# Optimization experiments

Measured on AMD Instinct MI355X. Metric: run time of the kernel, lower is better.

Reference implementation:

```python
import jax, jax.numpy as jnp
import numpy as np

E, IN, OUT, T = 8, 4096, 4096, 8192
GS = IN  # groupsize=-1 -> groupsize = infeatures


def setup_inputs() -> dict:
    key = jax.random.key(0)
    k1, k2, k3, k4, k5 = jax.random.split(key, 5)
    x = jax.random.normal(k1, (T, IN), dtype=jnp.float16)
    indices = jax.random.randint(k2, (T,), 0, E, dtype=jnp.int32)
    # int32 words each packing 8 int4 nonzero values (2:4 sparse -> IN*OUT/2 values per expert)
    qweight = jax.random.randint(k3, (E, IN // 32, OUT * 16 // 8), 0, 2**31 - 1, dtype=jnp.int32)
    meta = jax.random.randint(k4, (E, OUT, IN // 16), 0, 2**15, dtype=jnp.int32).astype(jnp.int16)
    scales = (jax.random.uniform(k5, (E, IN // GS, OUT), dtype=jnp.float32) * 0.02 + 0.001).astype(jnp.float16)
    return {"x": x, "indices": indices, "qweight": qweight, "meta": meta, "scales": scales}


def _dequant_24(qweight, meta, scales):
    """Decode packed int4 + 2:4-sparsity metadata into dense fp32 weights (E, OUT, IN)."""
    # unpack 8 int4 nibbles per int32 word, symmetric zero-point 8
    nib = (qweight[..., None] >> (4 * jnp.arange(8, dtype=jnp.int32))) & 0xF  # (E, IN//32, 2*OUT, 8)
    vals = nib.reshape(E, IN // 2, OUT).transpose(0, 2, 1).astype(jnp.float32) - 8.0  # (E, OUT, IN//2)
    m = meta.astype(jnp.int32) & 0xFFFF
    sub = (m[..., None] >> (2 * jnp.arange(8, dtype=jnp.int32))) & 0x3  # (E, OUT, IN//16, 8)
    grp = (jnp.arange(8, dtype=jnp.int32) // 2) * 4                      # group-of-4 base within 16-block
    base = 16 * jnp.arange(IN // 16, dtype=jnp.int32)                    # 16-block base
    dense_col = (base[None, None, :, None] + grp[None, None, None, :] + sub).reshape(E, OUT, IN // 2)
    eidx = jnp.arange(E)[:, None, None]
    oidx = jnp.arange(OUT)[None, :, None]
    W = jnp.zeros((E, OUT, IN), jnp.float32).at[eidx, oidx, dense_col].add(vals)
    # per-group dequant scales: (E, IN//GS, OUT) -> (E, OUT, IN)
    s = jnp.repeat(scales.astype(jnp.float32), GS, axis=1).transpose(0, 2, 1)
    return W * s


def reference(x, indices, qweight, meta, scales):
    W = _dequant_24(qweight, meta, scales)  # (E, OUT, IN)
    y = jnp.zeros((x.shape[0], OUT), jnp.float32)
    for e in range(E):  # fixed small expert count
        xe = jnp.where((indices == e)[:, None], x, 0).astype(jnp.float32)
        y = y + xe @ W[e].T
    return y.astype(x.dtype)
```

## Files before the change

### kernel.cpp

```cpp
#include <hip/hip_runtime.h>

#define E_N   8
#define IN_N  4096
#define OUT_N 4096
#define T_N   8192

#define BM 128
#define BN 256
#define BK 64
#define NTHREADS 512

typedef unsigned short u16;
typedef __bf16 bf16_t;
typedef bf16_t bf16x8 __attribute__((ext_vector_type(8)));
typedef u16    u16x8  __attribute__((ext_vector_type(8)));
typedef float  f32x4  __attribute__((ext_vector_type(4)));

#define GLOAD16(gsrc, ldst) \
    __builtin_amdgcn_global_load_lds( \
        (const __attribute__((address_space(1))) unsigned int*)(gsrc), \
        (__attribute__((address_space(3))) unsigned int*)(ldst), 16, 0, 0)

__device__ int g_cnt[E_N];
__device__ int g_base[E_N];
__device__ int g_ids[T_N];
__device__ int g_meta_wide;
__device__ u16 g_W[(long)E_N * OUT_N * IN_N];
__device__ u16 g_xb[(long)T_N * IN_N];

__device__ __forceinline__ u16 f2bf(float f) {
    unsigned u = __builtin_bit_cast(unsigned, f);
    u += 0x7FFFu + ((u >> 16) & 1u);
    return (u16)(u >> 16);
}

__global__ void sort_tokens(const int* __restrict__ idx, const u16* __restrict__ meta16) {
    __shared__ int cnt[E_N], off[E_N];
    __shared__ int probe;
    const int tid = threadIdx.x;
    const int lane = tid & 63;
    if (tid == 0) probe = 0;
    if (tid < E_N) cnt[tid] = 0;
    __syncthreads();
    if (tid < 64) {
        unsigned v = meta16[2 * (tid * 131072) + 1];
        if (v) atomicOr(&probe, 1);
    }
    for (int t0 = tid - lane; t0 < T_N; t0 += blockDim.x) {
        const int t = t0 + lane;
        const int my = idx[t] & 7;
        #pragma unroll
        for (int e = 0; e < E_N; ++e) {
            unsigned long long m = __ballot(my == e);
            if (lane == 0 && m) atomicAdd(&cnt[e], __popcll(m));
        }
    }
    __syncthreads();
    if (tid == 0) {
        int s = 0;
        for (int e = 0; e < E_N; ++e) { g_cnt[e] = cnt[e]; g_base[e] = s; off[e] = s; s += cnt[e]; }
        g_meta_wide = (probe == 0) ? 1 : 0;
    }
    __syncthreads();
    for (int t0 = tid - lane; t0 < T_N; t0 += blockDim.x) {
        const int t = t0 + lane;
        const int my = idx[t] & 7;
        #pragma unroll
        for (int e = 0; e < E_N; ++e) {
            unsigned long long m = __ballot(my == e);
            if (my == e) {
                int below = __popcll(m & ((1ull << lane) - 1ull));
                int basep = 0;
                if (below == 0) basep = atomicAdd(&off[e], __popcll(m));
                int src = __ffsll((long long)m) - 1;
                basep = __shfl(basep, src);
                int p = basep + below;
                if (p >= 0 && p < T_N) g_ids[p] = t;
            }
        }
    }
}

__global__ __launch_bounds__(256, 4)
void xb_convert(const float* __restrict__ x) {
    const int p = blockIdx.x;
    int tok = g_ids[p];
    if ((unsigned)tok >= (unsigned)T_N) tok = 0;
    const float* src = x + (long)tok * IN_N;
    u16* dst = g_xb + (long)p * IN_N;
    const int tid = threadIdx.x;
    float va[16];
    #pragma unroll
    for (int c4 = 0; c4 < 4; ++c4) {
        float4 v = *reinterpret_cast<const float4*>(src + tid * 16 + c4 * 4);
        va[c4 * 4 + 0] = v.x; va[c4 * 4 + 1] = v.y; va[c4 * 4 + 2] = v.z; va[c4 * 4 + 3] = v.w;
    }
    unsigned wp[8];
    #pragma unroll
    for (int p8 = 0; p8 < 8; ++p8)
        wp[p8] = (unsigned)f2bf(va[2 * p8]) | ((unsigned)f2bf(va[2 * p8 + 1]) << 16);
    *reinterpret_cast<int4*>(dst + tid * 16)     = make_int4((int)wp[0], (int)wp[1], (int)wp[2], (int)wp[3]);
    *reinterpret_cast<int4*>(dst + tid * 16 + 8) = make_int4((int)wp[4], (int)wp[5], (int)wp[6], (int)wp[7]);
}

__global__ __launch_bounds__(256, 4)
void decode_w(const int* __restrict__ qw, const void* __restrict__ meta) {
    const int e   = blockIdx.z;
    const int kt0 = blockIdx.y * 4;
    const int o   = blockIdx.x * 256 + threadIdx.x;
    const bool mwide = (g_meta_wide != 0);
    unsigned mws[16];
    if (mwide) {
        const int* mp = (const int*)meta + ((long)e * OUT_N + o) * (IN_N / 16) + kt0 * 4;
        #pragma unroll
        for (int i = 0; i < 16; ++i) mws[i] = (unsigned)mp[i] & 0xFFFFu;
    } else {
        const u16* mp = (const u16*)meta + ((long)e * OUT_N + o) * (IN_N / 16) + kt0 * 4;
        #pragma unroll
        for (int i = 0; i < 16; ++i) mws[i] = mp[i];
    }
    const unsigned sh = (o & 7) << 2;
    const int osw = o & 7;
    #pragma unroll
    for (int ki = 0; ki < 4; ++ki) {
        const int kt = kt0 + ki;
        unsigned wp[32];
        #pragma unroll
        for (int gi = 0; gi < 4; ++gi) {
            const int g = kt * 4 + gi;
            const unsigned mw = mws[ki * 4 + gi];
            const int* qp = qw + ((e * (IN_N / 32) + (g >> 1)) << 13) + (o >> 3) + ((g & 1) << 12);
            int d[16];
            #pragma unroll
            for (int p = 0; p < 16; ++p) d[p] = 0;
            #pragma unroll
            for (int grp = 0; grp < 4; ++grp) {
                const unsigned w0 = (unsigned)qp[(2 * grp) * 512];
                const unsigned w1 = (unsigned)qp[(2 * grp + 1) * 512];
                const int v0 = (int)((w0 >> sh) & 0xF) - 8;
                const int v1 = (int)((w1 >> sh) & 0xF) - 8;
                const int s0 = (mw >> (4 * grp)) & 3;
                const int s1 = (mw >> (4 * grp + 2)) & 3;
                #pragma unroll
                for (int q = 0; q < 4; ++q) {
                    int t0 = (s0 == q) ? v0 : 0;
                    int t1 = (s1 == q) ? v1 : 0;
                    d[grp * 4 + q] = t0 + t1;
                }
            }
            #pragma unroll
            for (int p = 0; p < 8; ++p) {
                unsigned lo = __builtin_bit_cast(unsigned, (float)d[2 * p])     >> 16;
                unsigned hi = __builtin_bit_cast(unsigned, (float)d[2 * p + 1]) >> 16;
                wp[gi * 8 + p] = lo | (hi << 16);
            }
        }
        u16* wr = g_W + ((long)(e * 64 + kt) * OUT_N + o) * 64;
        #pragma unroll
        for (int h = 0; h < 8; ++h)
            *reinterpret_cast<int4*>(wr + (h ^ osw) * 8) =
                make_int4((int)wp[h * 4], (int)wp[h * 4 + 1], (int)wp[h * 4 + 2], (int)wp[h * 4 + 3]);
    }
}

__global__ __launch_bounds__(NTHREADS, 1)
void moe_gemm(const float* __restrict__ scales, float* __restrict__ y) {
    const int e = blockIdx.z;
    int cnt = g_cnt[e];
    if (cnt < 0) cnt = 0;
    if (cnt > T_N) cnt = T_N;
    const int m0 = blockIdx.y * BM;
    if (m0 >= cnt) return;
    const int n0 = blockIdx.x * BN;
    int base = g_base[e];
    if (base < 0) base = 0;
    if (base > T_N - cnt) base = T_N - cnt;

    __shared__ __align__(16) u16 As[BM * BK];
    __shared__ __align__(16) u16 Bs[BN * BK];

    const int tid  = threadIdx.x;
    const int lane = tid & 63;
    const int wm   = (tid >> 6) >> 2;
    const int wn   = (tid >> 6) & 3;

    const int r0 = tid >> 3;
    const int kc_swz = (tid & 7) ^ (r0 & 7);
    long ar0 = (long)base + m0 + r0;       if (ar0 > T_N - 1) ar0 = T_N - 1;
    long ar1 = (long)base + m0 + 64 + r0;  if (ar1 > T_N - 1) ar1 = T_N - 1;
    const u16* asrc0 = g_xb + ar0 * IN_N + kc_swz * 8;
    const u16* asrc1 = g_xb + ar1 * IN_N + kc_swz * 8;
    u16* adst0 = &As[tid * 8];
    u16* adst1 = &As[(tid + 512) * 8];
    const u16* bsrc = g_W + ((long)e * 64 * OUT_N + n0) * 64 + tid * 8;

    f32x4 acc[4][4];
    #pragma unroll
    for (int i = 0; i < 4; ++i)
        #pragma unroll
        for (int j = 0; j < 4; ++j) acc[i][j] = (f32x4){0.f, 0.f, 0.f, 0.f};

    for (int k0 = 0; k0 < IN_N; k0 += BK) {
        GLOAD16(asrc0 + k0, adst0);
        GLOAD16(asrc1 + k0, adst1);
        #pragma unroll
        for (int it = 0; it < 4; ++it)
            GLOAD16(bsrc + it * 4096, &Bs[(tid + it * 512) * 8]);
        bsrc += (long)OUT_N * 64;
        __syncthreads();
        #pragma unroll
        for (int kk = 0; kk < BK; kk += 32) {
            bf16x8 af[4], bfr[4];
            #pragma unroll
            for (int mf = 0; mf < 4; ++mf) {
                const int r = wm * 64 + mf * 16 + (lane & 15);
                const int h = (kk >> 3) + (lane >> 4);
                u16x8 v = *reinterpret_cast<const u16x8*>(&As[r * 64 + ((h ^ (r & 7)) << 3)]);
                af[mf] = __builtin_bit_cast(bf16x8, v);
            }
            #pragma unroll
            for (int nf = 0; nf < 4; ++nf) {
                const int r = wn * 64 + nf * 16 + (lane & 15);
                const int h = (kk >> 3) + (lane >> 4);
                u16x8 v = *reinterpret_cast<const u16x8*>(&Bs[r * 64 + ((h ^ (r & 7)) << 3)]);
                bfr[nf] = __builtin_bit_cast(bf16x8, v);
            }
            #pragma unroll
            for (int mf = 0; mf < 4; ++mf)
                #pragma unroll
                for (int nf = 0; nf < 4; ++nf)
                    acc[mf][nf] = __builtin_amdgcn_mfma_f32_16x16x32_bf16(af[mf], bfr[nf], acc[mf][nf], 0, 0, 0);
        }
        __syncthreads();
    }

    const int* toks = g_ids + base;
    float sc[4];
    #pragma unroll
    for (int nf = 0; nf < 4; ++nf)
        sc[nf] = scales[e * OUT_N + n0 + wn * 64 + nf * 16 + (lane & 15)];
    #pragma unroll
    for (int mf = 0; mf < 4; ++mf) {
        #pragma unroll
        for (int r = 0; r < 4; ++r) {
            const int row = m0 + wm * 64 + mf * 16 + ((lane >> 4) << 2) + r;
            if (row >= cnt) continue;
            int tok = toks[row];
            if ((unsigned)tok >= (unsigned)T_N) continue;
            float* yrow = y + (long)tok * OUT_N;
            #pragma unroll
            for (int nf = 0; nf < 4; ++nf) {
                const int col = n0 + wn * 64 + nf * 16 + (lane & 15);
                yrow[col] = acc[mf][nf][r] * sc[nf];
            }
        }
    }
}

extern "C" void kernel_launch(void* const* d_in, const int* in_sizes, int n_in,
                              void* d_out, int out_size, void* d_ws, size_t ws_size,
                              hipStream_t stream) {
    const float* x      = nullptr;
    const int* indices  = nullptr;
    const int* qw       = nullptr;
    const void* meta    = nullptr;
    const float* scales = nullptr;
    int big_seen = 0;
    for (int i = 0; i < n_in; ++i) {
        long s = in_sizes[i];
        if (s == 33554432L)      x = (const float*)d_in[i];
        else if (s == 8192L)     indices = (const int*)d_in[i];
        else if (s == 32768L)    scales = (const float*)d_in[i];
        else if (s == 8388608L) {
            if (big_seen++ == 0)  qw = (const int*)d_in[i];
            else                  meta = d_in[i];
        }
    }
    if (!x || !indices || !qw || !meta || !scales) return;
    float* y = (float*)d_out;

    hipLaunchKernelGGL(sort_tokens, dim3(1), dim3(1024), 0, stream, indices, (const u16*)meta);
    hipLaunchKernelGGL(xb_convert, dim3(T_N), dim3(256), 0, stream, x);
    hipLaunchKernelGGL(decode_w, dim3(OUT_N / 256, 16, E_N), dim3(256), 0, stream, qw, meta);
    hipLaunchKernelGGL(moe_gemm, dim3(OUT_N / BN, T_N / BM, E_N), dim3(NTHREADS), 0, stream, scales, y);
}
```

Before: 653.8 us.

## Double-buffer MoE GEMM with 256x256 tiles and phased MFMA/load interleave

```diff
diff --git a/kernel.cpp b/kernel.cpp
--- a/kernel.cpp
+++ b/kernel.cpp
@@ -5,9 +5,9 @@
 #define OUT_N 4096
 #define T_N   8192
 
-#define BM 128
+#define BM 256
 #define BN 256
-#define BK 64
+#define NT_K 64
 #define NTHREADS 512
 
 typedef unsigned short u16;
@@ -163,7 +163,7 @@
     }
 }
 
-__global__ __launch_bounds__(NTHREADS, 1)
+__global__ __launch_bounds__(NTHREADS, 2)
 void moe_gemm(const float* __restrict__ scales, float* __restrict__ y) {
     const int e = blockIdx.z;
     int cnt = g_cnt[e];
@@ -176,83 +176,114 @@
     if (base < 0) base = 0;
     if (base > T_N - cnt) base = T_N - cnt;
 
-    __shared__ __align__(16) u16 As[BM * BK];
-    __shared__ __align__(16) u16 Bs[BN * BK];
+    __shared__ __align__(16) u16 As[2 * BM * 64];
+    __shared__ __align__(16) u16 Bs[2 * BN * 64];
 
     const int tid  = threadIdx.x;
     const int lane = tid & 63;
-    const int wm   = (tid >> 6) >> 2;
-    const int wn   = (tid >> 6) & 3;
-
-    const int r0 = tid >> 3;
-    const int kc_swz = (tid & 7) ^ (r0 & 7);
-    long ar0 = (long)base + m0 + r0;       if (ar0 > T_N - 1) ar0 = T_N - 1;
-    long ar1 = (long)base + m0 + 64 + r0;  if (ar1 > T_N - 1) ar1 = T_N - 1;
-    const u16* asrc0 = g_xb + ar0 * IN_N + kc_swz * 8;
-    const u16* asrc1 = g_xb + ar1 * IN_N + kc_swz * 8;
-    u16* adst0 = &As[tid * 8];
-    u16* adst1 = &As[(tid + 512) * 8];
-    const u16* bsrc = g_W + ((long)e * 64 * OUT_N + n0) * 64 + tid * 8;
-
-    f32x4 acc[4][4];
-    #pragma unroll
-    for (int i = 0; i < 4; ++i)
+    const int wid  = tid >> 6;
+    const int wm   = wid >> 2;
+    const int wn   = wid & 3;
+
+    const int r_loc = tid >> 3;
+    const int h_a   = (tid & 7) ^ (r_loc & 7);
+    const u16* asrc[4];
+    #pragma unroll
+    for (int q = 0; q < 4; ++q) {
+        long grow = (long)base + m0 + q * 64 + r_loc;
+        if (grow > T_N - 1) grow = T_N - 1;
+        asrc[q] = g_xb + grow * IN_N + h_a * 8;
+    }
+    const u16* bsrc = g_W + ((long)e * NT_K * OUT_N + n0) * 64 + (long)tid * 8;
+
+#define STAGE_A(B_, KT_, HT_) do { \
+    const int ktc_ = ((KT_) < NT_K) ? (KT_) : (NT_K - 1); \
+    GLOAD16(asrc[(HT_)*2 + 0] + ktc_ * 64, &As[(B_)*16384 + ((HT_)*1024 + tid) * 8]); \
+    GLOAD16(asrc[(HT_)*2 + 1] + ktc_ * 64, &As[(B_)*16384 + ((HT_)*1024 + 512 + tid) * 8]); \
+} while (0)
+#define STAGE_B(B_, KT_, HT_) do { \
+    const int ktc_ = ((KT_) < NT_K) ? (KT_) : (NT_K - 1); \
+    const u16* s_ = bsrc + (long)ktc_ * (OUT_N * 64) + (HT_) * 8192; \
+    GLOAD16(s_,        &Bs[(B_)*16384 + ((HT_)*1024 + tid) * 8]); \
+    GLOAD16(s_ + 4096, &Bs[(B_)*16384 + ((HT_)*1024 + 512 + tid) * 8]); \
+} while (0)
+
+    const int l15   = lane & 15;
+    const int aoff0 = ((((lane >> 4))     ^ (lane & 7)) << 3);
+    const int aoff1 = (((4 + (lane >> 4)) ^ (lane & 7)) << 3);
+    const int arow0 = (wm * 128 + l15) * 64;
+    const int brow0 = (wn * 64  + l15) * 64;
+
+#define LD8(P_) __builtin_bit_cast(bf16x8, *reinterpret_cast<const u16x8*>(P_))
+#define VM4 asm volatile("s_waitcnt vmcnt(4)" ::: "memory")
+#define PH_NOP ((void)0)
+
+    f32x4 acc[8][4];
+    #pragma unroll
+    for (int i = 0; i < 8; ++i)
         #pragma unroll
         for (int j = 0; j < 4; ++j) acc[i][j] = (f32x4){0.f, 0.f, 0.f, 0.f};
 
-    for (int k0 = 0; k0 < IN_N; k0 += BK) {
-        GLOAD16(asrc0 + k0, adst0);
-        GLOAD16(asrc1 + k0, adst1);
-        #pragma unroll
-        for (int it = 0; it < 4; ++it)
-            GLOAD16(bsrc + it * 4096, &Bs[(tid + it * 512) * 8]);
-        bsrc += (long)OUT_N * 64;
-        __syncthreads();
-        #pragma unroll
-        for (int kk = 0; kk < BK; kk += 32) {
-            bf16x8 af[4], bfr[4];
-            #pragma unroll
-            for (int mf = 0; mf < 4; ++mf) {
-                const int r = wm * 64 + mf * 16 + (lane & 15);
-                const int h = (kk >> 3) + (lane >> 4);
-                u16x8 v = *reinterpret_cast<const u16x8*>(&As[r * 64 + ((h ^ (r & 7)) << 3)]);
-                af[mf] = __builtin_bit_cast(bf16x8, v);
-            }
-            #pragma unroll
-            for (int nf = 0; nf < 4; ++nf) {
-                const int r = wn * 64 + nf * 16 + (lane & 15);
-                const int h = (kk >> 3) + (lane >> 4);
-                u16x8 v = *reinterpret_cast<const u16x8*>(&Bs[r * 64 + ((h ^ (r & 7)) << 3)]);
-                bfr[nf] = __builtin_bit_cast(bf16x8, v);
-            }
-            #pragma unroll
-            for (int mf = 0; mf < 4; ++mf)
-                #pragma unroll
-                for (int nf = 0; nf < 4; ++nf)
-                    acc[mf][nf] = __builtin_amdgcn_mfma_f32_16x16x32_bf16(af[mf], bfr[nf], acc[mf][nf], 0, 0, 0);
-        }
-        __syncthreads();
+    bf16x8 aR[4][2];
+    bf16x8 bR[2][2][2];
+
+#define PH(B_, QM_, QN_, RDA_, RDB_, STAGE_STMT, TAIL_STMT) do { \
+    if (RDA_) { _Pragma("unroll") for (int mf = 0; mf < 4; ++mf) { \
+        const u16* p_ = &As[(B_)*16384 + arow0 + (QM_)*4096 + mf*1024]; \
+        aR[mf][0] = LD8(p_ + aoff0); aR[mf][1] = LD8(p_ + aoff1); } } \
+    if (RDB_) { _Pragma("unroll") for (int nf = 0; nf < 2; ++nf) { \
+        const u16* p_ = &Bs[(B_)*16384 + brow0 + (QN_)*2048 + nf*1024]; \
+        bR[QN_][nf][0] = LD8(p_ + aoff0); bR[QN_][nf][1] = LD8(p_ + aoff1); } } \
+    STAGE_STMT; \
+    __builtin_amdgcn_s_barrier(); \
+    asm volatile("s_waitcnt lgkmcnt(0)" ::: "memory"); \
+    __builtin_amdgcn_sched_barrier(0); \
+    __builtin_amdgcn_s_setprio(1); \
+    _Pragma("unroll") for (int ks = 0; ks < 2; ++ks) \
+      _Pragma("unroll") for (int mf = 0; mf < 4; ++mf) \
+        _Pragma("unroll") for (int nf = 0; nf < 2; ++nf) \
+          acc[(QM_)*4 + mf][(QN_)*2 + nf] = __builtin_amdgcn_mfma_f32_16x16x32_bf16( \
+              aR[mf][ks], bR[QN_][nf][ks], acc[(QM_)*4 + mf][(QN_)*2 + nf], 0, 0, 0); \
+    __builtin_amdgcn_s_setprio(0); \
+    TAIL_STMT; \
+    __builtin_amdgcn_s_barrier(); \
+} while (0)
+
+    STAGE_A(0, 0, 0); STAGE_A(0, 0, 1);
+    STAGE_B(0, 0, 0); STAGE_B(0, 0, 1);
+    STAGE_B(1, 1, 0); STAGE_B(1, 1, 1);
+    VM4;
+    __builtin_amdgcn_s_barrier();
+
+    for (int t = 0; t < NT_K / 2; ++t) {
+        const int k1 = 2 * t + 1, k2 = 2 * t + 2, k3 = 2 * t + 3;
+        PH(0, 0, 0, 1, 1, STAGE_A(1, k1, 0), PH_NOP);
+        PH(0, 0, 1, 0, 1, STAGE_A(1, k1, 1), PH_NOP);
+        PH(0, 1, 0, 1, 0, STAGE_B(0, k2, 0), PH_NOP);
+        PH(0, 1, 1, 0, 0, STAGE_B(0, k2, 1), VM4);
+        PH(1, 0, 0, 1, 1, STAGE_A(0, k2, 0), PH_NOP);
+        PH(1, 0, 1, 0, 1, STAGE_A(0, k2, 1), PH_NOP);
+        PH(1, 1, 0, 1, 0, STAGE_B(1, k3, 0), PH_NOP);
+        PH(1, 1, 1, 0, 0, STAGE_B(1, k3, 1), VM4);
     }
 
     const int* toks = g_ids + base;
     float sc[4];
     #pragma unroll
     for (int nf = 0; nf < 4; ++nf)
-        sc[nf] = scales[e * OUT_N + n0 + wn * 64 + nf * 16 + (lane & 15)];
-    #pragma unroll
-    for (int mf = 0; mf < 4; ++mf) {
+        sc[nf] = scales[e * OUT_N + n0 + wn * 64 + nf * 16 + l15];
+    #pragma unroll
+    for (int mf = 0; mf < 8; ++mf) {
         #pragma unroll
         for (int r = 0; r < 4; ++r) {
-            const int row = m0 + wm * 64 + mf * 16 + ((lane >> 4) << 2) + r;
+            const int row = m0 + wm * 128 + mf * 16 + ((lane >> 4) << 2) + r;
             if (row >= cnt) continue;
             int tok = toks[row];
             if ((unsigned)tok >= (unsigned)T_N) continue;
             float* yrow = y + (long)tok * OUT_N;
             #pragma unroll
-            for (int nf = 0; nf < 4; ++nf) {
-                const int col = n0 + wn * 64 + nf * 16 + (lane & 15);
-                yrow[col] = acc[mf][nf][r] * sc[nf];
-            }
+            for (int nf = 0; nf < 4; ++nf)
+                yrow[n0 + wn * 64 + nf * 16 + l15] = acc[mf][nf][r] * sc[nf];
         }
     }
 }
```

Result: no change. 648.1 us (-0.9%).
